# Kernel tuning notes

Hardware: AMD Instinct MI355X
Metric: run time of the kernel (lower is better)

The kernel has to match this reference:

```python
import jax, jax.numpy as jnp
import numpy as np

MAX_REL = 128  # max_relative_position


def setup_inputs() -> dict:
    key = jax.random.key(0)
    k1, k2, k3, k4 = jax.random.split(key, 4)
    B, H, S, D = 2, 8, 2048, 64
    q = jax.random.normal(k1, (B, H, S, D), dtype=jnp.float32)
    k = jax.random.normal(k2, (B, H, S, D), dtype=jnp.float32)
    v = jax.random.normal(k3, (B, H, S, D), dtype=jnp.float32)
    rel_table = jax.random.normal(k4, (2 * MAX_REL + 1, D), dtype=jnp.float32)
    return {"q": q, "k": k, "v": v, "rel_table": rel_table}


def reference(q, k, v, rel_table):
    B, H, S, D = q.shape
    scale = jnp.sqrt(jnp.asarray(D, q.dtype))
    # content scores: [B,H,S,S]
    qk_scores = jnp.einsum('bhqd,bhkd->bhqk', q, k)
    # relative position index matrix [S,S] clamped to [-MAX_REL, MAX_REL]
    pos = jnp.arange(S)
    rel_idx = jnp.clip(pos[None, :] - pos[:, None], -MAX_REL, MAX_REL) + MAX_REL
    rel_emb = rel_table[rel_idx]  # [S,S,D]
    # relative scores: per-query dot with rel embedding row -> [B,H,S,S]
    rel_scores = jnp.einsum('bhqd,qkd->bhqk', q, rel_emb)
    scores = (qk_scores + rel_scores) / scale
    attn = jax.nn.softmax(scores, axis=-1)
    # output: [B,H,S,D]
    return jnp.einsum('bhqk,bhkd->bhqd', attn, v)
```

## Files before the change

### kernel.cpp

```cpp
#include <hip/hip_runtime.h>

typedef _Float16 half8 __attribute__((ext_vector_type(8)));
typedef _Float16 half4 __attribute__((ext_vector_type(4)));
typedef float f32x4 __attribute__((ext_vector_type(4)));

#define S_LEN 2048
#define HDIM 64
#define QBLK 64
#define KVBLK 64
#define NT (S_LEN / KVBLK)
#define QRS 258
#define NBH 16
#define L2E 1.44269504f
#define TSTR 72

__device__ __forceinline__ void load_lds16(const void* g, void* l) {
    __builtin_amdgcn_global_load_lds(
        (const __attribute__((address_space(1))) unsigned int*)g,
        (__attribute__((address_space(3))) unsigned int*)l, 16, 0, 0);
}

__global__ __launch_bounds__(256)
void convert_kv_kernel(const float* __restrict__ Kg, const float* __restrict__ Vg,
                       _Float16* __restrict__ Kh, _Float16* __restrict__ Vp)
{
    __shared__ _Float16 tile[KVBLK * TSTR];
    const int bid = blockIdx.x;
    const int tid = threadIdx.x;
    if (bid < 1024) {
        const int id = bid * 256 + tid;
        const int r  = id >> 3;
        const int d0 = (id & 7) * 8;
        const float* src = Kg + (size_t)r * HDIM + d0;
        f32x4 f0 = *(const f32x4*)(src);
        f32x4 f1 = *(const f32x4*)(src + 4);
        half8 h;
#pragma unroll
        for (int j = 0; j < 4; ++j) { h[j] = (_Float16)f0[j]; h[j+4] = (_Float16)f1[j]; }
        const int bh = r >> 11, kvg = r & 2047;
        const int t = kvg >> 6, kv = kvg & 63;
        const size_t blk = (size_t)(bh * NT + t) * 8192;
        const int off = (kv * 128 + d0 * 2) ^ ((kv & 7) << 4);
        *(half8*)((char*)Kh + blk + off) = h;
    } else {
        const int bt = bid - 1024;
        const int bh = bt >> 5, t = bt & 31;
        {
            const int kv = tid >> 2;
            const int d0 = (tid & 3) * 16;
            const float* src = Vg + ((size_t)bh * S_LEN + t * KVBLK + kv) * HDIM + d0;
            f32x4 f0 = *(const f32x4*)(src);
            f32x4 f1 = *(const f32x4*)(src + 4);
            f32x4 f2 = *(const f32x4*)(src + 8);
            f32x4 f3 = *(const f32x4*)(src + 12);
            half8 h0, h1;
#pragma unroll
            for (int j = 0; j < 4; ++j) {
                h0[j] = (_Float16)f0[j]; h0[j+4] = (_Float16)f1[j];
                h1[j] = (_Float16)f2[j]; h1[j+4] = (_Float16)f3[j];
            }
            *(half8*)&tile[kv * TSTR + d0]     = h0;
            *(half8*)&tile[kv * TSTR + d0 + 8] = h1;
        }
        __syncthreads();
        {
            const int dp = tid >> 2;
            const int u0 = (tid & 3) * 2;
            char* base = (char*)Vp + (size_t)bt * 8192;
            const int swz = (dp & 7) << 4;
#pragma unroll
            for (int ui = 0; ui < 2; ++ui) {
                const int u  = u0 + ui;
                const int kc = u >> 2, g = u & 3;
                half8 ch;
#pragma unroll
                for (int r = 0; r < 4; ++r) {
                    ch[r]     = tile[(32*kc + 4*g + r)      * TSTR + dp];
                    ch[4 + r] = tile[(32*kc + 16 + 4*g + r) * TSTR + dp];
                }
                *(half8*)(base + ((dp * 128 + u * 16) ^ swz)) = ch;
            }
        }
    }
}

__global__ __launch_bounds__(256, 2)
void relattn_v3(const float* __restrict__ Qg, const float* __restrict__ RELg,
                const _Float16* __restrict__ Kh, const _Float16* __restrict__ Vp,
                float* __restrict__ Og)
{
    __shared__ __attribute__((aligned(16))) _Float16 Kbuf[2][4096];
    __shared__ __attribute__((aligned(16))) _Float16 Vbuf[2][4096];
    __shared__ __attribute__((aligned(16))) _Float16 Qrel[QBLK * QRS];

    const int tid  = threadIdx.x;
    const int wave = tid >> 6;
    const int lane = tid & 63;
    const int c = lane & 15;
    const int g = lane >> 4;

    const int wk = ((blockIdx.x & 7) << 6) + (blockIdx.x >> 3);
    const int bh = wk >> 5;
    const int q0 = (wk & 31) * QBLK;

    const size_t hoff = (size_t)bh * S_LEN * HDIM;

    const int qg_ = q0 + wave * 16 + c;
    half8 aq[2];
#pragma unroll
    for (int kc = 0; kc < 2; ++kc) {
        const float* src = Qg + hoff + (size_t)qg_ * HDIM + kc * 32 + g * 8;
        f32x4 f0 = *(const f32x4*)(src);
        f32x4 f1 = *(const f32x4*)(src + 4);
        half8 h;
#pragma unroll
        for (int j = 0; j < 4; ++j) {
            h[j]     = (_Float16)(f0[j] * 0.125f);
            h[j + 4] = (_Float16)(f1[j] * 0.125f);
        }
        aq[kc] = h;
    }

#pragma unroll 1
    for (int t = 0; t < 17; ++t) {
        f32x4 acc = {0.f, 0.f, 0.f, 0.f};
        int r = t * 16 + c;
        if (r > 256) r = 256;
#pragma unroll
        for (int kc = 0; kc < 2; ++kc) {
            const float* src = RELg + (size_t)r * HDIM + kc * 32 + g * 8;
            f32x4 f0 = *(const f32x4*)(src);
            f32x4 f1 = *(const f32x4*)(src + 4);
            half8 b;
#pragma unroll
            for (int j = 0; j < 4; ++j) { b[j] = (_Float16)f0[j]; b[j+4] = (_Float16)f1[j]; }
            acc = __builtin_amdgcn_mfma_f32_16x16x32_f16(aq[kc], b, acc, 0, 0, 0);
        }
        const int col = t * 16 + c;
        if (col <= 256) {
#pragma unroll
            for (int reg = 0; reg < 4; ++reg)
                Qrel[(wave * 16 + 4 * g + reg) * QRS + col] = (_Float16)acc[reg];
        }
    }
    asm volatile("s_waitcnt lgkmcnt(0)" ::: "memory");
    const _Float16* qr = &Qrel[(wave * 16 + c) * QRS];
    const float bias_lo = (float)qr[0];
    const float bias_hi = (float)qr[256];

    const int swz  = (c & 7) << 4;
    const int off0 = (g * 16) ^ swz;
    const int off1 = (64 + g * 16) ^ swz;
    const char* kp0 = (const char*)Kbuf + c * 128 + off0;
    const char* kp1 = (const char*)Kbuf + c * 128 + off1;
    const char* vp0 = (const char*)Vbuf + c * 128 + off0;
    const char* vp1 = (const char*)Vbuf + c * 128 + off1;

    half8 ones;
#pragma unroll
    for (int j = 0; j < 8; ++j) ones[j] = (_Float16)1.0f;

    float m = -1e30f;
    f32x4 l_acc = {0.f, 0.f, 0.f, 0.f};
    f32x4 oacc[4];
#pragma unroll
    for (int i = 0; i < 4; ++i) oacc[i] = (f32x4){0.f, 0.f, 0.f, 0.f};

    const char* kbase = (const char*)Kh + (size_t)(bh * NT) * 8192;
    const char* vbase = (const char*)Vp + (size_t)(bh * NT) * 8192;
    const int goff = wave * 2048 + lane * 16;
    const int loff = wave * 2048;

#define ISSUE(tt, bb) do {                                              \
        const char* kt = kbase + (size_t)(tt) * 8192 + goff;            \
        const char* vt = vbase + (size_t)(tt) * 8192 + goff;            \
        char* kl = (char*)Kbuf + (bb) * 8192 + loff;                    \
        char* vl = (char*)Vbuf + (bb) * 8192 + loff;                    \
        load_lds16(kt,        kl);                                      \
        load_lds16(kt + 1024, kl + 1024);                               \
        load_lds16(vt,        vl);                                      \
        load_lds16(vt + 1024, vl + 1024);                               \
    } while (0)

#define BODY(t, b) do {                                                              \
        if ((t) + 1 < NT) {                                                          \
            ISSUE((t) + 1, (b) ^ 1);                                                 \
            asm volatile("s_waitcnt vmcnt(4)" ::: "memory");                         \
        } else {                                                                     \
            asm volatile("s_waitcnt vmcnt(0)" ::: "memory");                         \
        }                                                                            \
        __builtin_amdgcn_s_barrier();                                                \
        const int k0 = (t) * KVBLK;                                                  \
        f32x4 sacc[4];                                                               \
        _Pragma("unroll")                                                            \
        for (int n = 0; n < 4; ++n) sacc[n] = (f32x4){0.f,0.f,0.f,0.f};              \
        __builtin_amdgcn_s_setprio(1);                                               \
        _Pragma("unroll")                                                            \
        for (int n = 0; n < 4; ++n) {                                                \
            half8 ak0 = *(const half8*)(kp0 + (b) * 8192 + n * 2048);                \
            sacc[n] = __builtin_amdgcn_mfma_f32_16x16x32_f16(ak0, aq[0], sacc[n], 0, 0, 0); \
        }                                                                            \
        _Pragma("unroll")                                                            \
        for (int n = 0; n < 4; ++n) {                                                \
            half8 ak1 = *(const half8*)(kp1 + (b) * 8192 + n * 2048);                \
            sacc[n] = __builtin_amdgcn_mfma_f32_16x16x32_f16(ak1, aq[1], sacc[n], 0, 0, 0); \
        }                                                                            \
        __builtin_amdgcn_s_setprio(0);                                               \
        const bool band = (k0 + 192 > q0) && (k0 < q0 + 192);                        \
        float fold; float mtb;                                                       \
        if (!band) {                                                                 \
            const float bc = (k0 < q0) ? bias_lo : bias_hi;                          \
            float mt = sacc[0][0];                                                   \
            _Pragma("unroll")                                                        \
            for (int n = 0; n < 4; ++n)                                              \
                _Pragma("unroll")                                                    \
                for (int r = 0; r < 4; ++r) mt = fmaxf(mt, sacc[n][r]);              \
            mt = fmaxf(mt, __shfl_xor(mt, 16, 64));                                  \
            mt = fmaxf(mt, __shfl_xor(mt, 32, 64));                                  \
            mtb = mt + bc;                                                           \
            if (!__all(mtb <= m + 8.f)) {                                            \
                const float mnew = fmaxf(m, mtb);                                    \
                const float al = __builtin_amdgcn_exp2f((m - mnew) * L2E);           \
                m = mnew;                                                            \
                _Pragma("unroll")                                                    \
                for (int r = 0; r < 4; ++r) {                                        \
                    const float ar = __shfl(al, 20 * g + r, 64);                     \
                    l_acc[r] *= ar;                                                  \
                    _Pragma("unroll")                                                \
                    for (int dn = 0; dn < 4; ++dn) oacc[dn][r] *= ar;                \
                }                                                                    \
            }                                                                        \
            fold = (bc - m) * L2E;                                                   \
        } else {                                                                     \
            const int base_d = k0 + 4 * g - qg_ + 128;                               \
            float mt = -1e30f;                                                       \
            _Pragma("unroll")                                                        \
            for (int n = 0; n < 4; ++n) {                                            \
                _Pragma("unroll")                                                    \
                for (int r = 0; r < 4; ++r) {                                        \
                    int idx = base_d + 16 * n + r;                                   \
                    idx = idx < 0 ? 0 : (idx > 256 ? 256 : idx);                     \
                    sacc[n][r] += (float)qr[idx];                                    \
                    mt = fmaxf(mt, sacc[n][r]);                                      \
                }                                                                    \
            }                                                                        \
            mt = fmaxf(mt, __shfl_xor(mt, 16, 64));                                  \
            mt = fmaxf(mt, __shfl_xor(mt, 32, 64));                                  \
            mtb = mt;                                                                \
            if (!__all(mtb <= m + 8.f)) {                                            \
                const float mnew = fmaxf(m, mtb);                                    \
                const float al = __builtin_amdgcn_exp2f((m - mnew) * L2E);           \
                m = mnew;                                                            \
                _Pragma("unroll")                                                    \
                for (int r = 0; r < 4; ++r) {                                        \
                    const float ar = __shfl(al, 20 * g + r, 64);                     \
                    l_acc[r] *= ar;                                                  \
                    _Pragma("unroll")                                                \
                    for (int dn = 0; dn < 4; ++dn) oacc[dn][r] *= ar;                \
                }                                                                    \
            }                                                                        \
            fold = -m * L2E;                                                         \
        }                                                                            \
        half4 p4[4];                                                                 \
        _Pragma("unroll")                                                            \
        for (int n = 0; n < 4; ++n) {                                                \
            _Pragma("unroll")                                                        \
            for (int r = 0; r < 4; ++r) {                                            \
                const float pv = __builtin_amdgcn_exp2f(fmaf(sacc[n][r], L2E, fold));\
                p4[n][r] = (_Float16)pv;                                             \
            }                                                                        \
        }                                                                            \
        half8 ap0, ap1;                                                              \
        _Pragma("unroll")                                                            \
        for (int r = 0; r < 4; ++r) {                                                \
            ap0[r] = p4[0][r]; ap0[4 + r] = p4[1][r];                                \
            ap1[r] = p4[2][r]; ap1[4 + r] = p4[3][r];                                \
        }                                                                            \
        __builtin_amdgcn_s_setprio(1);                                               \
        l_acc = __builtin_amdgcn_mfma_f32_16x16x32_f16(ap0, ones, l_acc, 0, 0, 0);   \
        l_acc = __builtin_amdgcn_mfma_f32_16x16x32_f16(ap1, ones, l_acc, 0, 0, 0);   \
        _Pragma("unroll")                                                            \
        for (int dn = 0; dn < 4; ++dn) {                                             \
            half8 bv0 = *(const half8*)(vp0 + (b) * 8192 + dn * 2048);               \
            oacc[dn] = __builtin_amdgcn_mfma_f32_16x16x32_f16(ap0, bv0, oacc[dn], 0, 0, 0); \
        }                                                                            \
        _Pragma("unroll")                                                            \
        for (int dn = 0; dn < 4; ++dn) {                                             \
            half8 bv1 = *(const half8*)(vp1 + (b) * 8192 + dn * 2048);               \
            oacc[dn] = __builtin_amdgcn_mfma_f32_16x16x32_f16(ap1, bv1, oacc[dn], 0, 0, 0); \
        }                                                                            \
        __builtin_amdgcn_s_setprio(0);                                               \
        __builtin_amdgcn_s_barrier();                                                \
    } while (0)

    ISSUE(0, 0);
#pragma unroll 1
    for (int tt = 0; tt < NT; tt += 2) {
        BODY(tt, 0);
        BODY(tt + 1, 1);
    }
#undef BODY
#undef ISSUE

#pragma unroll
    for (int r = 0; r < 4; ++r) {
        const float inv = 1.0f / l_acc[r];
        float* dst = Og + hoff + (size_t)(q0 + wave * 16 + 4 * g + r) * HDIM + c;
#pragma unroll
        for (int dn = 0; dn < 4; ++dn)
            dst[16 * dn] = oacc[dn][r] * inv;
    }
}

__global__ __launch_bounds__(256, 2)
void relattn_v1(const float* __restrict__ Qg, const float* __restrict__ Kg,
                const float* __restrict__ Vg, const float* __restrict__ RELg,
                float* __restrict__ Og)
{
    __shared__ _Float16 Klds[KVBLK * HDIM];
    __shared__ _Float16 Vt[HDIM * KVBLK];
    __shared__ _Float16 Plds[4][16 * KVBLK];
    __shared__ _Float16 Qrel[QBLK * QRS];

    const int tid  = threadIdx.x;
    const int wave = tid >> 6;
    const int lane = tid & 63;
    const int c = lane & 15;
    const int g = lane >> 4;

    const int bid = blockIdx.x;
    const int bh  = bid >> 5;
    const int q0  = (bid & 31) * QBLK;

    const size_t hoff = (size_t)bh * S_LEN * HDIM;
    const float* Qh = Qg + hoff;
    const float* Kh = Kg + hoff;
    const float* Vh = Vg + hoff;

    const int qrow_frag = q0 + wave * 16 + c;
    half8 aq[2];
#pragma unroll
    for (int kc = 0; kc < 2; ++kc) {
        const float* src = Qh + (size_t)qrow_frag * HDIM + kc * 32 + g * 8;
        f32x4 f0 = *(const f32x4*)(src);
        f32x4 f1 = *(const f32x4*)(src + 4);
        half8 h;
#pragma unroll
        for (int j = 0; j < 4; ++j) {
            h[j]     = (_Float16)(f0[j] * 0.125f);
            h[j + 4] = (_Float16)(f1[j] * 0.125f);
        }
        aq[kc] = h;
    }

#pragma unroll 1
    for (int t = 0; t < 17; ++t) {
        f32x4 acc = {0.f, 0.f, 0.f, 0.f};
        int r = t * 16 + c;
        if (r > 256) r = 256;
#pragma unroll
        for (int kc = 0; kc < 2; ++kc) {
            const float* src = RELg + (size_t)r * HDIM + kc * 32 + g * 8;
            f32x4 f0 = *(const f32x4*)(src);
            f32x4 f1 = *(const f32x4*)(src + 4);
            half8 b;
#pragma unroll
            for (int j = 0; j < 4; ++j) { b[j] = (_Float16)f0[j]; b[j+4] = (_Float16)f1[j]; }
            acc = __builtin_amdgcn_mfma_f32_16x16x32_f16(aq[kc], b, acc, 0, 0, 0);
        }
        const int col = t * 16 + c;
        if (col <= 256) {
#pragma unroll
            for (int reg = 0; reg < 4; ++reg)
                Qrel[(wave * 16 + 4 * g + reg) * QRS + col] = (_Float16)acc[reg];
        }
    }

    float mrow[4], lrow[4];
    f32x4 oacc[4];
#pragma unroll
    for (int i = 0; i < 4; ++i) {
        mrow[i] = -1e30f; lrow[i] = 0.f;
        oacc[i] = (f32x4){0.f, 0.f, 0.f, 0.f};
    }

    for (int k0 = 0; k0 < S_LEN; k0 += KVBLK) {
        __syncthreads();
        {
            const int r  = tid >> 2;
            const int dq = (tid & 3) << 4;
            const float* src = Kh + (size_t)(k0 + r) * HDIM + dq;
            f32x4 f0 = *(const f32x4*)(src);
            f32x4 f1 = *(const f32x4*)(src + 4);
            f32x4 f2 = *(const f32x4*)(src + 8);
            f32x4 f3 = *(const f32x4*)(src + 12);
            half8 h0, h1;
#pragma unroll
            for (int j = 0; j < 4; ++j) {
                h0[j] = (_Float16)f0[j]; h0[j+4] = (_Float16)f1[j];
                h1[j] = (_Float16)f2[j]; h1[j+4] = (_Float16)f3[j];
            }
            const int swz = (r & 7) << 4;
            char* base = (char*)Klds;
            *(half8*)(base + ((r * 128 + dq * 2) ^ swz))      = h0;
            *(half8*)(base + ((r * 128 + dq * 2 + 16) ^ swz)) = h1;
        }
        {
            const int kv = tid & 63;
            const int dbase = (tid >> 6) << 4;
            const float* src = Vh + (size_t)(k0 + kv) * HDIM + dbase;
            f32x4 f0 = *(const f32x4*)(src);
            f32x4 f1 = *(const f32x4*)(src + 4);
            f32x4 f2 = *(const f32x4*)(src + 8);
            f32x4 f3 = *(const f32x4*)(src + 12);
            float vals[16];
#pragma unroll
            for (int j = 0; j < 4; ++j) {
                vals[j] = f0[j]; vals[4+j] = f1[j]; vals[8+j] = f2[j]; vals[12+j] = f3[j];
            }
            char* base = (char*)Vt;
#pragma unroll
            for (int i = 0; i < 16; ++i) {
                const int d = dbase + i;
                const int off = (d * 128 + kv * 2) ^ ((d & 7) << 4);
                *(_Float16*)(base + off) = (_Float16)vals[i];
            }
        }
        __syncthreads();

        f32x4 sacc[4];
#pragma unroll
        for (int n = 0; n < 4; ++n) sacc[n] = (f32x4){0.f,0.f,0.f,0.f};
#pragma unroll
        for (int kc = 0; kc < 2; ++kc) {
#pragma unroll
            for (int n = 0; n < 4; ++n) {
                const int off = (((16*n + c) * 128) + kc * 64 + g * 16) ^ ((c & 7) << 4);
                half8 bk = *(const half8*)((const char*)Klds + off);
                sacc[n] = __builtin_amdgcn_mfma_f32_16x16x32_f16(aq[kc], bk, sacc[n], 0, 0, 0);
            }
        }

        float sval[4][4];
        const int myq0 = q0 + wave * 16 + 4 * g;
#pragma unroll
        for (int n = 0; n < 4; ++n) {
            const int kpos = k0 + 16 * n + c;
#pragma unroll
            for (int reg = 0; reg < 4; ++reg) {
                int rel = kpos - (myq0 + reg);
                rel = rel < -128 ? -128 : (rel > 128 ? 128 : rel);
                const float bias = (float)Qrel[(wave*16 + 4*g + reg) * QRS + (rel + 128)];
                sval[n][reg] = sacc[n][reg] + bias;
            }
        }

        float mt[4];
#pragma unroll
        for (int reg = 0; reg < 4; ++reg) {
            float mp = fmaxf(fmaxf(sval[0][reg], sval[1][reg]),
                             fmaxf(sval[2][reg], sval[3][reg]));
#pragma unroll
            for (int msk = 1; msk < 16; msk <<= 1)
                mp = fmaxf(mp, __shfl_xor(mp, msk, 64));
            mt[reg] = mp;
        }

        float alpha[4], psum[4];
#pragma unroll
        for (int reg = 0; reg < 4; ++reg) {
            const float mn = fmaxf(mrow[reg], mt[reg]);
            alpha[reg] = __expf(mrow[reg] - mn);
            mrow[reg] = mn;
            psum[reg] = 0.f;
        }

        char* pbase = (char*)&Plds[wave][0];
#pragma unroll
        for (int n = 0; n < 4; ++n) {
#pragma unroll
            for (int reg = 0; reg < 4; ++reg) {
                const float pv = __expf(sval[n][reg] - mrow[reg]);
                psum[reg] += pv;
                const int row = 4 * g + reg;
                const int off = (row * 128 + (16 * n + c) * 2) ^ ((row & 7) << 4);
                *(_Float16*)(pbase + off) = (_Float16)pv;
            }
        }

#pragma unroll
        for (int reg = 0; reg < 4; ++reg) {
            float ps = psum[reg];
#pragma unroll
            for (int msk = 1; msk < 16; msk <<= 1)
                ps += __shfl_xor(ps, msk, 64);
            lrow[reg] = lrow[reg] * alpha[reg] + ps;
#pragma unroll
            for (int dn = 0; dn < 4; ++dn) oacc[dn][reg] *= alpha[reg];
        }

        asm volatile("s_waitcnt lgkmcnt(0)" ::: "memory");

        half8 ap[2];
#pragma unroll
        for (int kc = 0; kc < 2; ++kc) {
            const int off = (c * 128 + kc * 64 + g * 16) ^ ((c & 7) << 4);
            ap[kc] = *(const half8*)(pbase + off);
        }
#pragma unroll
        for (int kc = 0; kc < 2; ++kc) {
#pragma unroll
            for (int dn = 0; dn < 4; ++dn) {
                const int drow = 16 * dn + c;
                const int off = (drow * 128 + kc * 64 + g * 16) ^ ((c & 7) << 4);
                half8 bv = *(const half8*)((const char*)Vt + off);
                oacc[dn] = __builtin_amdgcn_mfma_f32_16x16x32_f16(ap[kc], bv, oacc[dn], 0, 0, 0);
            }
        }
    }

#pragma unroll
    for (int reg = 0; reg < 4; ++reg) {
        const float inv = 1.0f / lrow[reg];
        const int row = q0 + wave * 16 + 4 * g + reg;
        float* dst = Og + hoff + (size_t)row * HDIM + c;
#pragma unroll
        for (int dn = 0; dn < 4; ++dn)
            dst[16 * dn] = oacc[dn][reg] * inv;
    }
}

extern "C" void kernel_launch(void* const* d_in, const int* in_sizes, int n_in,
                              void* d_out, int out_size, void* d_ws, size_t ws_size,
                              hipStream_t stream) {
    const float* q   = (const float*)d_in[0];
    const float* k   = (const float*)d_in[1];
    const float* v   = (const float*)d_in[2];
    const float* rel = (const float*)d_in[3];
    float* out = (float*)d_out;
    (void)in_sizes; (void)n_in; (void)out_size;

    const size_t kv_bytes = (size_t)NBH * S_LEN * HDIM * sizeof(_Float16);
    if (ws_size >= 2 * kv_bytes) {
        _Float16* KhB = (_Float16*)d_ws;
        _Float16* VpB = (_Float16*)((char*)d_ws + kv_bytes);
        convert_kv_kernel<<<dim3(1536), 256, 0, stream>>>(k, v, KhB, VpB);
        relattn_v3<<<dim3(NBH * (S_LEN / QBLK)), 256, 0, stream>>>(q, rel, KhB, VpB, out);
    } else {
        relattn_v1<<<dim3(NBH * (S_LEN / QBLK)), 256, 0, stream>>>(q, k, v, rel, out);
    }
}
```

Measured before the change: 63.49 us.

## Split KV tile across two wave groups with LDS merge of partial softmax

Doubles the block to 512 threads. Each group of four waves handles half of every 64-key tile (32 keys), and the two partial softmax states are merged at the end through LDS. Only the first wave group computes the relative-position table, and each thread issues a single K and a single V async load per tile. The intent is more waves in flight for latency hiding and less serial work per wave. The cost is an fp16 round-trip of the partial outputs, extra barriers, and a loss of precision in the merge.

```diff
diff --git a/kernel.cpp b/kernel.cpp
--- a/kernel.cpp
+++ b/kernel.cpp
@@ -67,49 +67,52 @@
             const int dp = tid >> 2;
             const int u0 = (tid & 3) * 2;
             char* base = (char*)Vp + (size_t)bt * 8192;
-            const int swz = (dp & 7) << 4;
+            const int dsw = (dp & 7) << 4;
 #pragma unroll
             for (int ui = 0; ui < 2; ++ui) {
                 const int u  = u0 + ui;
-                const int kc = u >> 2, g = u & 3;
+                const int kc = u >> 2, gg = u & 3;
                 half8 ch;
 #pragma unroll
                 for (int r = 0; r < 4; ++r) {
-                    ch[r]     = tile[(32*kc + 4*g + r)      * TSTR + dp];
-                    ch[4 + r] = tile[(32*kc + 16 + 4*g + r) * TSTR + dp];
+                    ch[r]     = tile[(32*kc + 4*gg + r)      * TSTR + dp];
+                    ch[4 + r] = tile[(32*kc + 16 + 4*gg + r) * TSTR + dp];
                 }
-                *(half8*)(base + ((dp * 128 + u * 16) ^ swz)) = ch;
+                *(half8*)(base + ((dp * 128 + u * 16) ^ dsw)) = ch;
             }
         }
     }
 }
 
-__global__ __launch_bounds__(256, 2)
-void relattn_v3(const float* __restrict__ Qg, const float* __restrict__ RELg,
+__global__ __launch_bounds__(512, 4)
+void relattn_v7(const float* __restrict__ Qg, const float* __restrict__ RELg,
                 const _Float16* __restrict__ Kh, const _Float16* __restrict__ Vp,
                 float* __restrict__ Og)
 {
     __shared__ __attribute__((aligned(16))) _Float16 Kbuf[2][4096];
     __shared__ __attribute__((aligned(16))) _Float16 Vbuf[2][4096];
     __shared__ __attribute__((aligned(16))) _Float16 Qrel[QBLK * QRS];
+    __shared__ float MLds[2][64];
+    __shared__ float LLds[2][64];
 
     const int tid  = threadIdx.x;
     const int wave = tid >> 6;
     const int lane = tid & 63;
-    const int c = lane & 15;
-    const int g = lane >> 4;
+    const int c  = lane & 15;
+    const int g  = lane >> 4;
+    const int qs = wave & 3;
+    const int ks = wave >> 2;
 
     const int wk = ((blockIdx.x & 7) << 6) + (blockIdx.x >> 3);
     const int bh = wk >> 5;
     const int q0 = (wk & 31) * QBLK;
-
     const size_t hoff = (size_t)bh * S_LEN * HDIM;
 
-    const int qg_ = q0 + wave * 16 + c;
-    half8 aq[2];
+    const int qb0 = q0 + 16 * qs;
+    half8 bq[2];
 #pragma unroll
     for (int kc = 0; kc < 2; ++kc) {
-        const float* src = Qg + hoff + (size_t)qg_ * HDIM + kc * 32 + g * 8;
+        const float* src = Qg + hoff + (size_t)(qb0 + c) * HDIM + kc * 32 + g * 8;
         f32x4 f0 = *(const f32x4*)(src);
         f32x4 f1 = *(const f32x4*)(src + 4);
         half8 h;
@@ -118,43 +121,55 @@
             h[j]     = (_Float16)(f0[j] * 0.125f);
             h[j + 4] = (_Float16)(f1[j] * 0.125f);
         }
-        aq[kc] = h;
-    }
-
+        bq[kc] = h;
+    }
+
+    if (ks == 0) {
 #pragma unroll 1
-    for (int t = 0; t < 17; ++t) {
-        f32x4 acc = {0.f, 0.f, 0.f, 0.f};
-        int r = t * 16 + c;
-        if (r > 256) r = 256;
-#pragma unroll
-        for (int kc = 0; kc < 2; ++kc) {
-            const float* src = RELg + (size_t)r * HDIM + kc * 32 + g * 8;
-            f32x4 f0 = *(const f32x4*)(src);
-            f32x4 f1 = *(const f32x4*)(src + 4);
-            half8 b;
-#pragma unroll
-            for (int j = 0; j < 4; ++j) { b[j] = (_Float16)f0[j]; b[j+4] = (_Float16)f1[j]; }
-            acc = __builtin_amdgcn_mfma_f32_16x16x32_f16(aq[kc], b, acc, 0, 0, 0);
-        }
-        const int col = t * 16 + c;
-        if (col <= 256) {
-#pragma unroll
-            for (int reg = 0; reg < 4; ++reg)
-                Qrel[(wave * 16 + 4 * g + reg) * QRS + col] = (_Float16)acc[reg];
-        }
-    }
-    asm volatile("s_waitcnt lgkmcnt(0)" ::: "memory");
-    const _Float16* qr = &Qrel[(wave * 16 + c) * QRS];
+        for (int t = 0; t < 17; ++t) {
+            f32x4 acc = {0.f, 0.f, 0.f, 0.f};
+            int r = t * 16 + c;
+            if (r > 256) r = 256;
+#pragma unroll
+            for (int kc = 0; kc < 2; ++kc) {
+                const float* src = RELg + (size_t)r * HDIM + kc * 32 + g * 8;
+                f32x4 f0 = *(const f32x4*)(src);
+                f32x4 f1 = *(const f32x4*)(src + 4);
+                half8 b;
+#pragma unroll
+                for (int j = 0; j < 4; ++j) { b[j] = (_Float16)f0[j]; b[j+4] = (_Float16)f1[j]; }
+                acc = __builtin_amdgcn_mfma_f32_16x16x32_f16(bq[kc], b, acc, 0, 0, 0);
+            }
+            const int col = t * 16 + c;
+            if (col <= 256) {
+#pragma unroll
+                for (int reg = 0; reg < 4; ++reg)
+                    Qrel[(16 * qs + 4 * g + reg) * QRS + col] = (_Float16)acc[reg];
+            }
+        }
+    }
+
+    const char* kimg = (const char*)Kh + (size_t)bh * NT * 8192;
+    const char* vimg = (const char*)Vp + (size_t)bh * NT * 8192;
+    load_lds16(kimg + tid * 16, (char*)Kbuf + tid * 16);
+    load_lds16(vimg + tid * 16, (char*)Vbuf + tid * 16);
+
+    __syncthreads();
+
+    const _Float16* qr = &Qrel[(16 * qs + c) * QRS];
     const float bias_lo = (float)qr[0];
     const float bias_hi = (float)qr[256];
 
-    const int swz  = (c & 7) << 4;
-    const int off0 = (g * 16) ^ swz;
-    const int off1 = (64 + g * 16) ^ swz;
-    const char* kp0 = (const char*)Kbuf + c * 128 + off0;
-    const char* kp1 = (const char*)Kbuf + c * 128 + off1;
-    const char* vp0 = (const char*)Vbuf + c * 128 + off0;
-    const char* vp1 = (const char*)Vbuf + c * 128 + off1;
+    const int swz = (c & 7) << 4;
+    int akoff[2][2], voff[4];
+#pragma unroll
+    for (int n = 0; n < 2; ++n)
+#pragma unroll
+        for (int kc = 0; kc < 2; ++kc)
+            akoff[n][kc] = (((32 * ks + 16 * n + c) * 128) + kc * 64 + g * 16) ^ swz;
+#pragma unroll
+    for (int dn = 0; dn < 4; ++dn)
+        voff[dn] = (((16 * dn + c) * 128) + ks * 64 + g * 16) ^ swz;
 
     half8 ones;
 #pragma unroll
@@ -166,149 +181,139 @@
 #pragma unroll
     for (int i = 0; i < 4; ++i) oacc[i] = (f32x4){0.f, 0.f, 0.f, 0.f};
 
-    const char* kbase = (const char*)Kh + (size_t)(bh * NT) * 8192;
-    const char* vbase = (const char*)Vp + (size_t)(bh * NT) * 8192;
-    const int goff = wave * 2048 + lane * 16;
-    const int loff = wave * 2048;
-
-#define ISSUE(tt, bb) do {                                              \
-        const char* kt = kbase + (size_t)(tt) * 8192 + goff;            \
-        const char* vt = vbase + (size_t)(tt) * 8192 + goff;            \
-        char* kl = (char*)Kbuf + (bb) * 8192 + loff;                    \
-        char* vl = (char*)Vbuf + (bb) * 8192 + loff;                    \
-        load_lds16(kt,        kl);                                      \
-        load_lds16(kt + 1024, kl + 1024);                               \
-        load_lds16(vt,        vl);                                      \
-        load_lds16(vt + 1024, vl + 1024);                               \
-    } while (0)
-
 #define BODY(t, b) do {                                                              \
-        if ((t) + 1 < NT) {                                                          \
-            ISSUE((t) + 1, (b) ^ 1);                                                 \
-            asm volatile("s_waitcnt vmcnt(4)" ::: "memory");                         \
+        asm volatile("s_waitcnt vmcnt(0)" ::: "memory");                             \
+        __builtin_amdgcn_s_barrier();                                                \
+        {                                                                            \
+            const int tn = ((t) + 1 < NT) ? (t) + 1 : (t);                           \
+            load_lds16(kimg + (size_t)tn * 8192 + tid * 16,                          \
+                       (char*)Kbuf + ((b) ^ 1) * 8192 + tid * 16);                   \
+            load_lds16(vimg + (size_t)tn * 8192 + tid * 16,                          \
+                       (char*)Vbuf + ((b) ^ 1) * 8192 + tid * 16);                   \
+        }                                                                            \
+        const char* kb = (const char*)Kbuf + (b) * 8192;                             \
+        const char* vb = (const char*)Vbuf + (b) * 8192;                             \
+        const int kws = (t) * KVBLK + 32 * ks;                                       \
+        half8 a00 = *(const half8*)(kb + akoff[0][0]);                               \
+        half8 a01 = *(const half8*)(kb + akoff[0][1]);                               \
+        half8 a10 = *(const half8*)(kb + akoff[1][0]);                               \
+        half8 a11 = *(const half8*)(kb + akoff[1][1]);                               \
+        f32x4 s0 = {0.f,0.f,0.f,0.f}, s1 = {0.f,0.f,0.f,0.f};                        \
+        __builtin_amdgcn_s_setprio(1);                                               \
+        s0 = __builtin_amdgcn_mfma_f32_16x16x32_f16(a00, bq[0], s0, 0, 0, 0);        \
+        s1 = __builtin_amdgcn_mfma_f32_16x16x32_f16(a10, bq[0], s1, 0, 0, 0);        \
+        s0 = __builtin_amdgcn_mfma_f32_16x16x32_f16(a01, bq[1], s0, 0, 0, 0);        \
+        s1 = __builtin_amdgcn_mfma_f32_16x16x32_f16(a11, bq[1], s1, 0, 0, 0);        \
+        __builtin_amdgcn_s_setprio(0);                                               \
+        float bias = 0.f;                                                            \
+        float lm;                                                                    \
+        if (kws + 159 <= qb0) {                                                      \
+            bias = bias_lo;                                                          \
+            lm = fmaxf(fmaxf(fmaxf(s0[0], s0[1]), fmaxf(s0[2], s0[3])),              \
+                       fmaxf(fmaxf(s1[0], s1[1]), fmaxf(s1[2], s1[3]))) + bias;      \
+        } else if (kws >= qb0 + 143) {                                               \
+            bias = bias_hi;                                                          \
+            lm = fmaxf(fmaxf(fmaxf(s0[0], s0[1]), fmaxf(s0[2], s0[3])),              \
+                       fmaxf(fmaxf(s1[0], s1[1]), fmaxf(s1[2], s1[3]))) + bias;      \
         } else {                                                                     \
-            asm volatile("s_waitcnt vmcnt(0)" ::: "memory");                         \
+            const int base_d = kws + 4 * g - (qb0 + c) + 128;                        \
+            _Pragma("unroll")                                                        \
+            for (int r = 0; r < 4; ++r) {                                            \
+                int i0 = base_d + r;                                                 \
+                i0 = i0 < 0 ? 0 : (i0 > 256 ? 256 : i0);                             \
+                int i1 = base_d + 16 + r;                                            \
+                i1 = i1 < 0 ? 0 : (i1 > 256 ? 256 : i1);                             \
+                s0[r] += (float)qr[i0];                                              \
+                s1[r] += (float)qr[i1];                                              \
+            }                                                                        \
+            lm = fmaxf(fmaxf(fmaxf(s0[0], s0[1]), fmaxf(s0[2], s0[3])),              \
+                       fmaxf(fmaxf(s1[0], s1[1]), fmaxf(s1[2], s1[3])));             \
         }                                                                            \
-        __builtin_amdgcn_s_barrier();                                                \
-        const int k0 = (t) * KVBLK;                                                  \
-        f32x4 sacc[4];                                                               \
-        _Pragma("unroll")                                                            \
-        for (int n = 0; n < 4; ++n) sacc[n] = (f32x4){0.f,0.f,0.f,0.f};              \
-        __builtin_amdgcn_s_setprio(1);                                               \
-        _Pragma("unroll")                                                            \
-        for (int n = 0; n < 4; ++n) {                                                \
-            half8 ak0 = *(const half8*)(kp0 + (b) * 8192 + n * 2048);                \
-            sacc[n] = __builtin_amdgcn_mfma_f32_16x16x32_f16(ak0, aq[0], sacc[n], 0, 0, 0); \
-        }                                                                            \
-        _Pragma("unroll")                                                            \
-        for (int n = 0; n < 4; ++n) {                                                \
-            half8 ak1 = *(const half8*)(kp1 + (b) * 8192 + n * 2048);                \
-            sacc[n] = __builtin_amdgcn_mfma_f32_16x16x32_f16(ak1, aq[1], sacc[n], 0, 0, 0); \
-        }                                                                            \
-        __builtin_amdgcn_s_setprio(0);                                               \
-        const bool band = (k0 + 192 > q0) && (k0 < q0 + 192);                        \
-        float fold; float mtb;                                                       \
-        if (!band) {                                                                 \
-            const float bc = (k0 < q0) ? bias_lo : bias_hi;                          \
-            float mt = sacc[0][0];                                                   \
-            _Pragma("unroll")                                                        \
-            for (int n = 0; n < 4; ++n)                                              \
-                _Pragma("unroll")                                                    \
-                for (int r = 0; r < 4; ++r) mt = fmaxf(mt, sacc[n][r]);              \
+        if (!__all(lm <= m + 8.f)) {                                                 \
+            float mt = lm;                                                           \
             mt = fmaxf(mt, __shfl_xor(mt, 16, 64));                                  \
             mt = fmaxf(mt, __shfl_xor(mt, 32, 64));                                  \
-            mtb = mt + bc;                                                           \
-            if (!__all(mtb <= m + 8.f)) {                                            \
-                const float mnew = fmaxf(m, mtb);                                    \
-                const float al = __builtin_amdgcn_exp2f((m - mnew) * L2E);           \
-                m = mnew;                                                            \
-                _Pragma("unroll")                                                    \
-                for (int r = 0; r < 4; ++r) {                                        \
-                    const float ar = __shfl(al, 20 * g + r, 64);                     \
-                    l_acc[r] *= ar;                                                  \
-                    _Pragma("unroll")                                                \
-                    for (int dn = 0; dn < 4; ++dn) oacc[dn][r] *= ar;                \
-                }                                                                    \
-            }                                                                        \
-            fold = (bc - m) * L2E;                                                   \
-        } else {                                                                     \
-            const int base_d = k0 + 4 * g - qg_ + 128;                               \
-            float mt = -1e30f;                                                       \
-            _Pragma("unroll")                                                        \
-            for (int n = 0; n < 4; ++n) {                                            \
-                _Pragma("unroll")                                                    \
-                for (int r = 0; r < 4; ++r) {                                        \
-                    int idx = base_d + 16 * n + r;                                   \
-                    idx = idx < 0 ? 0 : (idx > 256 ? 256 : idx);                     \
-                    sacc[n][r] += (float)qr[idx];                                    \
-                    mt = fmaxf(mt, sacc[n][r]);                                      \
-                }                                                                    \
-            }                                                                        \
-            mt = fmaxf(mt, __shfl_xor(mt, 16, 64));                                  \
-            mt = fmaxf(mt, __shfl_xor(mt, 32, 64));                                  \
-            mtb = mt;                                                                \
-            if (!__all(mtb <= m + 8.f)) {                                            \
-                const float mnew = fmaxf(m, mtb);                                    \
-                const float al = __builtin_amdgcn_exp2f((m - mnew) * L2E);           \
-                m = mnew;                                                            \
-                _Pragma("unroll")                                                    \
-                for (int r = 0; r < 4; ++r) {                                        \
-                    const float ar = __shfl(al, 20 * g + r, 64);                     \
-                    l_acc[r] *= ar;                                                  \
-                    _Pragma("unroll")                                                \
-                    for (int dn = 0; dn < 4; ++dn) oacc[dn][r] *= ar;                \
-                }                                                                    \
-            }                                                                        \
-            fold = -m * L2E;                                                         \
-        }                                                                            \
-        half4 p4[4];                                                                 \
-        _Pragma("unroll")                                                            \
-        for (int n = 0; n < 4; ++n) {                                                \
+            const float mnew = fmaxf(m, mt);                                         \
+            const float al = __builtin_amdgcn_exp2f((m - mnew) * L2E);               \
+            m = mnew;                                                                \
             _Pragma("unroll")                                                        \
             for (int r = 0; r < 4; ++r) {                                            \
-                const float pv = __builtin_amdgcn_exp2f(fmaf(sacc[n][r], L2E, fold));\
-                p4[n][r] = (_Float16)pv;                                             \
+                const float ar = __shfl(al, 20 * g + r, 64);                         \
+                l_acc[r] *= ar;                                                      \
+                _Pragma("unroll")                                                    \
+                for (int dn = 0; dn < 4; ++dn) oacc[dn][r] *= ar;                    \
             }                                                                        \
         }                                                                            \
-        half8 ap0, ap1;                                                              \
+        const float fold = (bias - m) * L2E;                                         \
+        half8 ap;                                                                    \
         _Pragma("unroll")                                                            \
         for (int r = 0; r < 4; ++r) {                                                \
-            ap0[r] = p4[0][r]; ap0[4 + r] = p4[1][r];                                \
-            ap1[r] = p4[2][r]; ap1[4 + r] = p4[3][r];                                \
+            ap[r]     = (_Float16)__builtin_amdgcn_exp2f(fmaf(s0[r], L2E, fold));    \
+            ap[4 + r] = (_Float16)__builtin_amdgcn_exp2f(fmaf(s1[r], L2E, fold));    \
         }                                                                            \
+        half8 v0 = *(const half8*)(vb + voff[0]);                                    \
+        half8 v1 = *(const half8*)(vb + voff[1]);                                    \
+        half8 v2 = *(const half8*)(vb + voff[2]);                                    \
+        half8 v3 = *(const half8*)(vb + voff[3]);                                    \
         __builtin_amdgcn_s_setprio(1);                                               \
-        l_acc = __builtin_amdgcn_mfma_f32_16x16x32_f16(ap0, ones, l_acc, 0, 0, 0);   \
-        l_acc = __builtin_amdgcn_mfma_f32_16x16x32_f16(ap1, ones, l_acc, 0, 0, 0);   \
-        _Pragma("unroll")                                                            \
-        for (int dn = 0; dn < 4; ++dn) {                                             \
-            half8 bv0 = *(const half8*)(vp0 + (b) * 8192 + dn * 2048);               \
-            oacc[dn] = __builtin_amdgcn_mfma_f32_16x16x32_f16(ap0, bv0, oacc[dn], 0, 0, 0); \
-        }                                                                            \
-        _Pragma("unroll")                                                            \
-        for (int dn = 0; dn < 4; ++dn) {                                             \
-            half8 bv1 = *(const half8*)(vp1 + (b) * 8192 + dn * 2048);               \
-            oacc[dn] = __builtin_amdgcn_mfma_f32_16x16x32_f16(ap1, bv1, oacc[dn], 0, 0, 0); \
-        }                                                                            \
+        l_acc   = __builtin_amdgcn_mfma_f32_16x16x32_f16(ap, ones, l_acc, 0, 0, 0);  \
+        oacc[0] = __builtin_amdgcn_mfma_f32_16x16x32_f16(ap, v0, oacc[0], 0, 0, 0);  \
+        oacc[1] = __builtin_amdgcn_mfma_f32_16x16x32_f16(ap, v1, oacc[1], 0, 0, 0);  \
+        oacc[2] = __builtin_amdgcn_mfma_f32_16x16x32_f16(ap, v2, oacc[2], 0, 0, 0);  \
+        oacc[3] = __builtin_amdgcn_mfma_f32_16x16x32_f16(ap, v3, oacc[3], 0, 0, 0);  \
         __builtin_amdgcn_s_setprio(0);                                               \
-        __builtin_amdgcn_s_barrier();                                                \
     } while (0)
 
-    ISSUE(0, 0);
 #pragma unroll 1
     for (int tt = 0; tt < NT; tt += 2) {
         BODY(tt, 0);
         BODY(tt + 1, 1);
     }
 #undef BODY
-#undef ISSUE
-
-#pragma unroll
-    for (int r = 0; r < 4; ++r) {
-        const float inv = 1.0f / l_acc[r];
-        float* dst = Og + hoff + (size_t)(q0 + wave * 16 + 4 * g + r) * HDIM + c;
-#pragma unroll
-        for (int dn = 0; dn < 4; ++dn)
-            dst[16 * dn] = oacc[dn][r] * inv;
+
+    asm volatile("s_waitcnt vmcnt(0)" ::: "memory");
+    __syncthreads();
+
+    {
+        char* Ob = (char*)Kbuf;
+#pragma unroll
+        for (int r = 0; r < 4; ++r) {
+            const int row = 16 * qs + 4 * g + r;
+            const int rsw = (row & 7) << 4;
+#pragma unroll
+            for (int dn = 0; dn < 4; ++dn)
+                *(_Float16*)(Ob + ks * 8192 + ((row * 128 + (16 * dn + c) * 2) ^ rsw))
+                    = (_Float16)oacc[dn][r];
+        }
+        if (g == 0) MLds[ks][16 * qs + c] = m;
+        if (c == 0) {
+#pragma unroll
+            for (int r = 0; r < 4; ++r)
+                LLds[ks][16 * qs + 4 * g + r] = l_acc[r];
+        }
+        __syncthreads();
+
+        const int row = 16 * qs + c;
+        const int rsw = (c & 7) << 4;
+        const float m0 = MLds[0][row], m1 = MLds[1][row];
+        const float l0 = LLds[0][row], l1 = LLds[1][row];
+        const float M  = fmaxf(m0, m1);
+        const float w0 = __builtin_amdgcn_exp2f((m0 - M) * L2E);
+        const float w1 = __builtin_amdgcn_exp2f((m1 - M) * L2E);
+        const float inv = 1.0f / (l0 * w0 + l1 * w1);
+
+        const int dof = 64 * ks + 16 * g;
+        half8 o0 = *(const half8*)(Ob +        ((row * 128 + dof) ^ rsw));
+        half8 o1 = *(const half8*)(Ob + 8192 + ((row * 128 + dof) ^ rsw));
+        float* dst = Og + hoff + (size_t)(q0 + row) * HDIM + 32 * ks + 8 * g;
+        f32x4 oA, oB;
+#pragma unroll
+        for (int j = 0; j < 4; ++j) {
+            oA[j] = ((float)o0[j]     * w0 + (float)o1[j]     * w1) * inv;
+            oB[j] = ((float)o0[4 + j] * w0 + (float)o1[4 + j] * w1) * inv;
+        }
+        *(f32x4*)dst = oA;
+        *(f32x4*)(dst + 4) = oB;
     }
 }
 
@@ -545,7 +550,7 @@
         _Float16* KhB = (_Float16*)d_ws;
         _Float16* VpB = (_Float16*)((char*)d_ws + kv_bytes);
         convert_kv_kernel<<<dim3(1536), 256, 0, stream>>>(k, v, KhB, VpB);
-        relattn_v3<<<dim3(NBH * (S_LEN / QBLK)), 256, 0, stream>>>(q, rel, KhB, VpB, out);
+        relattn_v7<<<dim3(NBH * (S_LEN / QBLK)), 512, 0, stream>>>(q, rel, KhB, VpB, out);
     } else {
         relattn_v1<<<dim3(NBH * (S_LEN / QBLK)), 256, 0, stream>>>(q, k, v, rel, out);
     }
```

Measured after the change: 58.59 us, median of 2. 7.7% less time.
